# Kernel tuning notes

Measured on AMD Instinct MI355X. Metric: run time of the kernel, lower is better.

Reference implementation:

```python
import jax, jax.numpy as jnp
import numpy as np

EMBED_DIM = 1024
NUM_HEADS = 16
HEAD_DIM = EMBED_DIM // NUM_HEADS
MAX_DIST = 128
NUM_BUCKETS = 2 * MAX_DIST + 1  # 257: fixes off-by-one in original Embedding sizing


def setup_inputs() -> dict:
    key = jax.random.key(0)
    ks = jax.random.split(key, 10)
    B, S, D = 2, 2048, EMBED_DIM
    s = 1.0 / np.sqrt(D)
    return {
        "x": jax.random.normal(ks[0], (B, S, D), dtype=jnp.float32),
        "Wq": jax.random.normal(ks[1], (D, D), dtype=jnp.float32) * s,
        "bq": jnp.zeros((D,), dtype=jnp.float32),
        "Wk": jax.random.normal(ks[2], (D, D), dtype=jnp.float32) * s,
        "bk": jnp.zeros((D,), dtype=jnp.float32),
        "Wv": jax.random.normal(ks[3], (D, D), dtype=jnp.float32) * s,
        "bv": jnp.zeros((D,), dtype=jnp.float32),
        "Wo": jax.random.normal(ks[4], (D, D), dtype=jnp.float32) * s,
        "bo": jnp.zeros((D,), dtype=jnp.float32),
        "rel_emb": jax.random.normal(ks[5], (NUM_BUCKETS, NUM_HEADS), dtype=jnp.float32) * 0.02,
    }


def _rel_bias(rel_emb, seq_len):
    # relative position clamped to [-MAX_DIST, MAX_DIST], shifted to [0, 2*MAX_DIST]
    pos = jnp.arange(seq_len)
    rel = jnp.clip(pos[:, None] - pos[None, :], -MAX_DIST, MAX_DIST) + MAX_DIST
    bias = rel_emb[rel]                    # [S, S, H]
    return jnp.transpose(bias, (2, 0, 1))  # [H, S, S]


def reference(x, Wq, bq, Wk, bk, Wv, bv, Wo, bo, rel_emb):
    B, S, D = x.shape
    H, Hd = NUM_HEADS, HEAD_DIM
    # torch Linear: y = x @ W.T + b
    q = (x @ Wq.T + bq).reshape(B, S, H, Hd).transpose(0, 2, 1, 3)  # [B,H,S,Hd]
    k = (x @ Wk.T + bk).reshape(B, S, H, Hd).transpose(0, 2, 1, 3)
    v = (x @ Wv.T + bv).reshape(B, S, H, Hd).transpose(0, 2, 1, 3)
    scores = jnp.einsum("bhqd,bhkd->bhqk", q, k) / jnp.sqrt(jnp.float32(Hd))
    scores = scores + _rel_bias(rel_emb, S)[None]  # add [H,S,S] bias
    probs = jax.nn.softmax(scores, axis=-1)
    out = jnp.einsum("bhqk,bhkd->bhqd", probs, v)
    out = out.transpose(0, 2, 1, 3).reshape(B, S, D)
    return out @ Wo.T + bo
```

## Files before the change

kernel.cpp:

```cpp
#include <hip/hip_runtime.h>
#include <hip/hip_bf16.h>
#include <cstdint>
#include <cstddef>

#define DEVI __device__ __forceinline__

static constexpr int SEQ = 2048;
static constexpr int DM  = 1024;
static constexpr int NH  = 16;
static constexpr int HD  = 64;
static constexpr int NTOK = 2 * SEQ;
static constexpr int NBUCKET = 257;
static constexpr float LOG2E = 1.44269504088896f;

typedef __attribute__((ext_vector_type(8))) short bf16x8;
typedef __attribute__((ext_vector_type(4))) float f32x4;
#define MFMA16(a, b, c) __builtin_amdgcn_mfma_f32_16x16x32_bf16((a), (b), (c), 0, 0, 0)

DEVI float bf1(uint16_t u)  { return __uint_as_float(((uint32_t)u) << 16); }
DEVI uint16_t f2bf(float f) {
    uint32_t x = __float_as_uint(f);
    x += 0x7fffu + ((x >> 16) & 1u);
    return (uint16_t)(x >> 16);
}
DEVI bf16x8 ld_frag(const uint16_t* p) {
    union { uint4 u; bf16x8 f; } c;
    c.u = *(const uint4*)p;
    return c.f;
}
DEVI void gld16(const uint16_t* g, uint16_t* l) {
    __builtin_amdgcn_global_load_lds(
        (const __attribute__((address_space(1))) uint32_t*)g,
        (__attribute__((address_space(3))) uint32_t*)l, 16, 0, 0);
}

__global__ void sniff_kernel(const uint16_t* __restrict__ x, int* __restrict__ flag)
{
    int bad = 0;
    for (int i = threadIdx.x; i < 512; i += 64) {
        const float v = bf1(x[i]);
        if (!(fabsf(v) < 64.0f)) bad = 1;
    }
    const unsigned long long m = __ballot(bad);
    if (threadIdx.x == 0) *flag = (m != 0ull) ? 1 : 0;
}

__global__ __launch_bounds__(256)
void convert_kernel(const void* __restrict__ x, const void* __restrict__ Wq,
                    const void* __restrict__ Wk, const void* __restrict__ Wv,
                    const void* __restrict__ Wo, const void* __restrict__ bq,
                    const void* __restrict__ bk, const void* __restrict__ bv,
                    const void* __restrict__ bo, uint16_t* __restrict__ dst,
                    const int* __restrict__ flagp)
{
    const bool f32in = (*flagp != 0);
    const size_t M4 = 4194304, M1 = 1048576;
    const size_t e = ((size_t)blockIdx.x * 256 + threadIdx.x) * 8;
    const void* src; size_t off;
    if      (e < M4)                 { src = x;  off = e; }
    else if (e < M4 + M1)            { src = Wq; off = e - M4; }
    else if (e < M4 + 2*M1)          { src = Wk; off = e - M4 - M1; }
    else if (e < M4 + 3*M1)          { src = Wv; off = e - M4 - 2*M1; }
    else if (e < M4 + 4*M1)          { src = Wo; off = e - M4 - 3*M1; }
    else if (e < M4 + 4*M1 + 1024)   { src = bq; off = e - M4 - 4*M1; }
    else if (e < M4 + 4*M1 + 2048)   { src = bk; off = e - M4 - 4*M1 - 1024; }
    else if (e < M4 + 4*M1 + 3072)   { src = bv; off = e - M4 - 4*M1 - 2048; }
    else                             { src = bo; off = e - M4 - 4*M1 - 3072; }
    if (f32in) {
        const float4 a = *(const float4*)((const float*)src + off);
        const float4 b = *(const float4*)((const float*)src + off + 4);
        uint4 o;
        o.x = (uint32_t)f2bf(a.x) | ((uint32_t)f2bf(a.y) << 16);
        o.y = (uint32_t)f2bf(a.z) | ((uint32_t)f2bf(a.w) << 16);
        o.z = (uint32_t)f2bf(b.x) | ((uint32_t)f2bf(b.y) << 16);
        o.w = (uint32_t)f2bf(b.z) | ((uint32_t)f2bf(b.w) << 16);
        *(uint4*)(dst + e) = o;
    } else {
        *(uint4*)(dst + e) = *(const uint4*)((const uint16_t*)src + off);
    }
}

__global__ __launch_bounds__(256)
void gemm_qkv(const uint16_t* __restrict__ xc, const uint16_t* __restrict__ Wqkv,
              const uint16_t* __restrict__ bqkv,
              uint16_t* __restrict__ Qw, uint16_t* __restrict__ Kw,
              uint16_t* __restrict__ Vt)
{
    __shared__ uint16_t As[128 * 32];
    __shared__ uint16_t Bs[128 * 32];
    const int tid = threadIdx.x, bx = blockIdx.x;
    const int lane = tid & 63, wave = tid >> 6;
    const int ln = lane & 15, quad = lane >> 4;
    const int wm = (wave & 1) * 64, wn = (wave >> 1) * 64;

    const uint16_t *Ab, *Bb;
    int bm, bn, vor;
    if (bx < 512) {
        vor = 0; bm = (bx >> 4) * 128; bn = (bx & 15) * 128;
        Ab = xc + (size_t)bm * DM;  Bb = Wqkv + (size_t)bn * DM;
    } else {
        vor = 1; const int b2 = bx - 512; bm = (b2 >> 5) * 128; bn = (b2 & 31) * 128;
        Ab = Wqkv + (size_t)(2048 + bm) * DM;  Bb = xc + (size_t)bn * DM;
    }

    f32x4 acc[4][4];
    #pragma unroll
    for (int i = 0; i < 4; ++i)
        #pragma unroll
        for (int j = 0; j < 4; ++j) acc[i][j] = (f32x4){0.f, 0.f, 0.f, 0.f};

    const int s0 = tid, s1 = 256 + tid;
    const uint16_t* ga0 = Ab + (size_t)(s0 >> 2) * DM + (s0 & 3) * 8;
    const uint16_t* ga1 = Ab + (size_t)(s1 >> 2) * DM + (s1 & 3) * 8;
    const uint16_t* gb0 = Bb + (size_t)(s0 >> 2) * DM + (s0 & 3) * 8;
    const uint16_t* gb1 = Bb + (size_t)(s1 >> 2) * DM + (s1 & 3) * 8;

    for (int k0 = 0; k0 < DM; k0 += 32) {
        __syncthreads();
        gld16(ga0 + k0, &As[s0 * 8]);
        gld16(ga1 + k0, &As[s1 * 8]);
        gld16(gb0 + k0, &Bs[s0 * 8]);
        gld16(gb1 + k0, &Bs[s1 * 8]);
        __syncthreads();

        bf16x8 af[4], bfr[4];
        #pragma unroll
        for (int t = 0; t < 4; ++t) {
            af[t]  = ld_frag(&As[(wm + t * 16 + ln) * 32 + quad * 8]);
            bfr[t] = ld_frag(&Bs[(wn + t * 16 + ln) * 32 + quad * 8]);
        }
        #pragma unroll
        for (int ti = 0; ti < 4; ++ti)
            #pragma unroll
            for (int tj = 0; tj < 4; ++tj)
                acc[ti][tj] = MFMA16(af[ti], bfr[tj], acc[ti][tj]);
    }

    if (!vor) {
        #pragma unroll
        for (int tj = 0; tj < 4; ++tj) {
            const int c = bn + wn + tj * 16 + ln;
            const int mat = c >> 10, h = (c >> 6) & 15, hd = c & 63;
            uint16_t* dstp = mat ? Kw : Qw;
            const float scale = mat ? 1.0f : (0.125f * LOG2E);
            const float bb = bf1(bqkv[c]);
            #pragma unroll
            for (int ti = 0; ti < 4; ++ti)
                #pragma unroll
                for (int r = 0; r < 4; ++r) {
                    const int row = bm + wm + ti * 16 + quad * 4 + r;
                    const int b = row >> 11, s = row & 2047;
                    dstp[(((size_t)b * NH + h) * SEQ + s) * HD + hd] =
                        f2bf((acc[ti][tj][r] + bb) * scale);
                }
        }
    } else {
        #pragma unroll
        for (int ti = 0; ti < 4; ++ti)
            #pragma unroll
            for (int r = 0; r < 4; ++r) {
                const int f = bm + wm + ti * 16 + quad * 4 + r;
                const int h = f >> 6, hd = f & 63;
                const float bb = bf1(bqkv[2048 + f]);
                #pragma unroll
                for (int tj = 0; tj < 4; ++tj) {
                    const int t = bn + wn + tj * 16 + ln;
                    const int b = t >> 11, s = t & 2047;
                    Vt[(((size_t)b * NH + h) * HD + hd) * SEQ + s] = f2bf(acc[ti][tj][r] + bb);
                }
            }
    }
}

__global__ __launch_bounds__(256)
void gemm_out(const uint16_t* __restrict__ Cw, const uint16_t* __restrict__ Woc,
              const uint16_t* __restrict__ boc, void* __restrict__ out,
              const int* __restrict__ flagp)
{
    __shared__ uint16_t As[128 * 32];
    __shared__ uint16_t Bs[64 * 32];
    const int tid = threadIdx.x, bx = blockIdx.x;
    const int lane = tid & 63, wave = tid >> 6;
    const int ln = lane & 15, quad = lane >> 4;
    const int wm = (wave & 1) * 64, wn = (wave >> 1) * 32;
    const int bm = (bx >> 4) * 128, bn = (bx & 15) * 64;
    const uint16_t* Ab = Cw + (size_t)bm * DM;
    const uint16_t* Bb = Woc + (size_t)bn * DM;

    f32x4 acc[4][2];
    #pragma unroll
    for (int i = 0; i < 4; ++i)
        #pragma unroll
        for (int j = 0; j < 2; ++j) acc[i][j] = (f32x4){0.f, 0.f, 0.f, 0.f};

    const int s0 = tid, s1 = 256 + tid;
    const uint16_t* ga0 = Ab + (size_t)(s0 >> 2) * DM + (s0 & 3) * 8;
    const uint16_t* ga1 = Ab + (size_t)(s1 >> 2) * DM + (s1 & 3) * 8;
    const uint16_t* gb0 = Bb + (size_t)(s0 >> 2) * DM + (s0 & 3) * 8;

    for (int k0 = 0; k0 < DM; k0 += 32) {
        __syncthreads();
        gld16(ga0 + k0, &As[s0 * 8]);
        gld16(ga1 + k0, &As[s1 * 8]);
        gld16(gb0 + k0, &Bs[s0 * 8]);
        __syncthreads();

        bf16x8 af[4], bfr[2];
        #pragma unroll
        for (int t = 0; t < 4; ++t)
            af[t] = ld_frag(&As[(wm + t * 16 + ln) * 32 + quad * 8]);
        #pragma unroll
        for (int t = 0; t < 2; ++t)
            bfr[t] = ld_frag(&Bs[(wn + t * 16 + ln) * 32 + quad * 8]);
        #pragma unroll
        for (int ti = 0; ti < 4; ++ti)
            #pragma unroll
            for (int tj = 0; tj < 2; ++tj)
                acc[ti][tj] = MFMA16(af[ti], bfr[tj], acc[ti][tj]);
    }

    const bool f32o = (*flagp != 0);
    #pragma unroll
    for (int tj = 0; tj < 2; ++tj) {
        const int c = bn + wn + tj * 16 + ln;
        const float bb = bf1(boc[c]);
        #pragma unroll
        for (int ti = 0; ti < 4; ++ti)
            #pragma unroll
            for (int r = 0; r < 4; ++r) {
                const int row = bm + wm + ti * 16 + quad * 4 + r;
                const float v = acc[ti][tj][r] + bb;
                if (f32o) ((float*)out)[(size_t)row * DM + c] = v;
                else      ((uint16_t*)out)[(size_t)row * DM + c] = f2bf(v);
            }
    }
}

__global__ __launch_bounds__(256)
void attn_mfma(const uint16_t* __restrict__ Q, const uint16_t* __restrict__ K,
               const uint16_t* __restrict__ Vt, const void* __restrict__ rel,
               uint16_t* __restrict__ ctx, const int* __restrict__ flagp)
{
    __shared__ alignas(16) uint16_t Ks[64 * 64];
    __shared__ alignas(16) uint16_t Vls[64 * 64];
    __shared__ alignas(16) uint16_t Pl[4][16 * 64];
    __shared__ float bias_s[NBUCKET];

    const bool f32in = (*flagp != 0);
    const int tid = threadIdx.x, wave = tid >> 6, lane = tid & 63;
    const int ln = lane & 15, quad = lane >> 4;

    const int blk = blockIdx.x;
    const int bh = (blk & 7) * 4 + ((blk >> 3) & 3);
    const int qt = blk >> 5;
    const int b = bh >> 4, h = bh & 15;
    const int q0 = qt * 64;

    for (int i = tid; i < NBUCKET; i += 256) {
        const float bv = f32in ? ((const float*)rel)[i * NH + h]
                               : bf1(((const uint16_t*)rel)[i * NH + h]);
        bias_s[i] = bv * LOG2E;
    }
    __syncthreads();
    const float bneg = bias_s[0], bpos = bias_s[256];
    const float C8 = 8.0f * LOG2E;

    const uint16_t* qp = Q + ((size_t)bh * SEQ + q0 + wave * 16 + ln) * HD;
    const bf16x8 qf0 = ld_frag(qp + quad * 8);
    const bf16x8 qf1 = ld_frag(qp + 32 + quad * 8);

    f32x4 o[4];
    float lacc = 0.f;
    #pragma unroll
    for (int dt = 0; dt < 4; ++dt) o[dt] = (f32x4){0.f, 0.f, 0.f, 0.f};

    const uint16_t* Kb  = K  + (size_t)bh * SEQ * HD;
    const uint16_t* Vtb = Vt + (size_t)bh * HD * SEQ;
    const int swz = ln & 7;
    uint16_t* myP = Pl[wave];

    for (int k0 = 0; k0 < SEQ; k0 += 64) {
        __syncthreads();
        #pragma unroll
        for (int it = 0; it < 2; ++it) {
            const int s = it * 256 + tid;
            const int row = s >> 3, p = s & 7, c = p ^ (row & 7);
            gld16(Kb + (size_t)(k0 + row) * HD + c * 8, &Ks[s * 8]);
        }
        #pragma unroll
        for (int it = 0; it < 2; ++it) {
            const int s = it * 256 + tid;
            const int row = s >> 3, p = s & 7, c = p ^ (row & 7);
            gld16(Vtb + (size_t)row * SEQ + k0 + c * 8, &Vls[s * 8]);
        }
        __syncthreads();

        const int mode = (k0 >= q0 + 192) ? 0 : ((k0 + 192 <= q0) ? 2 : 1);
        const float bcst = ((mode == 0) ? bneg : bpos) - C8;

        #pragma unroll
        for (int nt = 0; nt < 4; ++nt) {
            const int krow = (nt * 16 + ln) * 64;
            const bf16x8 kf0 = ld_frag(&Ks[krow + ((0 + quad) ^ swz) * 8]);
            const bf16x8 kf1 = ld_frag(&Ks[krow + ((4 + quad) ^ swz) * 8]);
            f32x4 s4 = (f32x4){0.f, 0.f, 0.f, 0.f};
            s4 = MFMA16(kf0, qf0, s4);
            s4 = MFMA16(kf1, qf1, s4);
            uint32_t pb[4];
            #pragma unroll
            for (int r = 0; r < 4; ++r) {
                float sv;
                if (mode != 1) {
                    sv = s4[r] + bcst;
                } else {
                    const int kk = k0 + nt * 16 + quad * 4 + r;
                    const int qq = q0 + wave * 16 + ln;
                    int dd = qq - kk;
                    dd = min(128, max(-128, dd)) + 128;
                    sv = s4[r] + bias_s[dd] - C8;
                }
                pb[r] = __float_as_uint(exp2f(sv)) & 0xffff0000u;
                lacc += __uint_as_float(pb[r]);
            }
            const uint2 dw = {__builtin_amdgcn_perm(pb[1], pb[0], 0x07060302u),
                              __builtin_amdgcn_perm(pb[3], pb[2], 0x07060302u)};
            const int cb = (2 * nt + (quad >> 1)) ^ swz;
            *(uint2*)&myP[ln * 64 + cb * 8 + (quad & 1) * 4] = dw;
        }
        bf16x8 pf[2];
        #pragma unroll
        for (int kc = 0; kc < 2; ++kc)
            pf[kc] = ld_frag(&myP[ln * 64 + ((kc * 4 + quad) ^ swz) * 8]);
        #pragma unroll
        for (int dt = 0; dt < 4; ++dt) {
            const int vrow = (dt * 16 + ln) * 64;
            #pragma unroll
            for (int kc = 0; kc < 2; ++kc) {
                const bf16x8 vf = ld_frag(&Vls[vrow + ((kc * 4 + quad) ^ swz) * 8]);
                o[dt] = MFMA16(pf[kc], vf, o[dt]);
            }
        }
    }

    float lr = lacc;
    lr += __shfl_xor(lr, 16);
    lr += __shfl_xor(lr, 32);
    const float linv = 1.0f / lr;
    #pragma unroll
    for (int r = 0; r < 4; ++r) {
        const float inv_r = __shfl(linv, quad * 4 + r);
        const int qq = q0 + wave * 16 + quad * 4 + r;
        #pragma unroll
        for (int dt = 0; dt < 4; ++dt) {
            const float v = o[dt][r] * inv_r;
            ctx[(((size_t)b * SEQ + qq) * NH + h) * HD + dt * 16 + ln] = f2bf(v);
        }
    }
}

extern "C" void kernel_launch(void* const* d_in, const int* in_sizes, int n_in,
                              void* d_out, int out_size, void* d_ws, size_t ws_size,
                              hipStream_t stream)
{
    const void* x   = d_in[0];
    const void* Wq  = d_in[1];
    const void* bq  = d_in[2];
    const void* Wk  = d_in[3];
    const void* bk  = d_in[4];
    const void* Wv  = d_in[5];
    const void* bv  = d_in[6];
    const void* Wo  = d_in[7];
    const void* bo  = d_in[8];
    const void* rel = d_in[9];

    const size_t M4 = 4194304, M1 = 1048576;
    uint16_t* ws16 = (uint16_t*)d_ws;
    uint16_t* xc   = ws16;
    uint16_t* Wqkv = ws16 + M4;
    uint16_t* Woc  = ws16 + M4 + 3 * M1;
    uint16_t* bqkv = ws16 + M4 + 4 * M1;
    uint16_t* boc  = bqkv + 3072;
    uint16_t* Qw   = ws16 + M4 + 4 * M1 + 8192;
    uint16_t* Kw   = Qw + M4;
    uint16_t* Vt   = Kw + M4;
    int* flag = (int*)(Vt + M4);
    uint16_t* Cw = xc;

    sniff_kernel<<<1, 64, 0, stream>>>((const uint16_t*)x, flag);
    convert_kernel<<<4098, 256, 0, stream>>>(x, Wq, Wk, Wv, Wo, bq, bk, bv, bo,
                                             ws16, flag);
    gemm_qkv<<<768, 256, 0, stream>>>(xc, Wqkv, bqkv, Qw, Kw, Vt);
    attn_mfma<<<1024, 256, 0, stream>>>(Qw, Kw, Vt, rel, Cw, flag);
    gemm_out<<<512, 256, 0, stream>>>(Cw, Woc, boc, d_out, flag);
}
```

Measured before the change: 239.6 us.

## Compute softmax row sums via MFMA with ones vector and fold bias into accumulator init

Replaces the per-element scalar row-sum accumulation and its final cross-lane shuffles with two extra MFMAs per tile that multiply the stored bf16 probabilities by a ones vector. The constant bias and offset are folded into the MFMA accumulator initialisation and the bias table, removing per-element adds. The clamped-bias path is specialised into its own branch, and all LDS and global address arithmetic is hoisted out of the key loop. It also sets a minimum-blocks-per-SM hint in launch bounds, which may constrain register allocation.

```diff
diff --git a/kernel.cpp b/kernel.cpp
--- a/kernel.cpp
+++ b/kernel.cpp
@@ -236,7 +236,7 @@
     }
 }
 
-__global__ __launch_bounds__(256)
+__global__ __launch_bounds__(256, 4)
 void attn_mfma(const uint16_t* __restrict__ Q, const uint16_t* __restrict__ K,
                const uint16_t* __restrict__ Vt, const void* __restrict__ rel,
                uint16_t* __restrict__ ctx, const int* __restrict__ flagp)
@@ -256,21 +256,25 @@
     const int b = bh >> 4, h = bh & 15;
     const int q0 = qt * 64;
 
+    const float C8 = 8.0f * LOG2E;
     for (int i = tid; i < NBUCKET; i += 256) {
         const float bv = f32in ? ((const float*)rel)[i * NH + h]
                                : bf1(((const uint16_t*)rel)[i * NH + h]);
-        bias_s[i] = bv * LOG2E;
+        bias_s[i] = bv * LOG2E - C8;
     }
     __syncthreads();
     const float bneg = bias_s[0], bpos = bias_s[256];
-    const float C8 = 8.0f * LOG2E;
 
     const uint16_t* qp = Q + ((size_t)bh * SEQ + q0 + wave * 16 + ln) * HD;
     const bf16x8 qf0 = ld_frag(qp + quad * 8);
     const bf16x8 qf1 = ld_frag(qp + 32 + quad * 8);
 
+    union { uint4 u; bf16x8 f; } onec;
+    onec.u = (uint4){0x3F803F80u, 0x3F803F80u, 0x3F803F80u, 0x3F803F80u};
+    const bf16x8 onef = onec.f;
+
     f32x4 o[4];
-    float lacc = 0.f;
+    f32x4 lf = (f32x4){0.f, 0.f, 0.f, 0.f};
     #pragma unroll
     for (int dt = 0; dt < 4; ++dt) o[dt] = (f32x4){0.f, 0.f, 0.f, 0.f};
 
@@ -279,82 +283,107 @@
     const int swz = ln & 7;
     uint16_t* myP = Pl[wave];
 
+    const int s_0 = tid, s_1 = 256 + tid;
+    const int r_0 = s_0 >> 3, c_0 = (s_0 & 7) ^ (r_0 & 7);
+    const int r_1 = s_1 >> 3, c_1 = (s_1 & 7) ^ (r_1 & 7);
+    const int koff0 = r_0 * HD + c_0 * 8,  koff1 = r_1 * HD + c_1 * 8;
+    const int voff0 = r_0 * SEQ + c_0 * 8, voff1 = r_1 * SEQ + c_1 * 8;
+    uint16_t* const kl0 = &Ks[s_0 * 8];
+    uint16_t* const kl1 = &Ks[s_1 * 8];
+    uint16_t* const vl0 = &Vls[s_0 * 8];
+    uint16_t* const vl1 = &Vls[s_1 * 8];
+
+    const uint16_t* kfp[4][2];
+    const uint16_t* vfp[4][2];
+    #pragma unroll
+    for (int t = 0; t < 4; ++t) {
+        const int row = (t * 16 + ln) * 64;
+        kfp[t][0] = &Ks[row + ((0 + quad) ^ swz) * 8];
+        kfp[t][1] = &Ks[row + ((4 + quad) ^ swz) * 8];
+        vfp[t][0] = &Vls[row + ((0 + quad) ^ swz) * 8];
+        vfp[t][1] = &Vls[row + ((4 + quad) ^ swz) * 8];
+    }
+    uint16_t* Pw[4];
+    #pragma unroll
+    for (int nt = 0; nt < 4; ++nt) {
+        const int cb = (2 * nt + (quad >> 1)) ^ swz;
+        Pw[nt] = &myP[ln * 64 + cb * 8 + (quad & 1) * 4];
+    }
+    const uint16_t* const pfp0 = &myP[ln * 64 + ((0 + quad) ^ swz) * 8];
+    const uint16_t* const pfp1 = &myP[ln * 64 + ((4 + quad) ^ swz) * 8];
+
+    const uint16_t* kgb = Kb;
+    const uint16_t* vgb = Vtb;
+
     for (int k0 = 0; k0 < SEQ; k0 += 64) {
         __syncthreads();
-        #pragma unroll
-        for (int it = 0; it < 2; ++it) {
-            const int s = it * 256 + tid;
-            const int row = s >> 3, p = s & 7, c = p ^ (row & 7);
-            gld16(Kb + (size_t)(k0 + row) * HD + c * 8, &Ks[s * 8]);
-        }
-        #pragma unroll
-        for (int it = 0; it < 2; ++it) {
-            const int s = it * 256 + tid;
-            const int row = s >> 3, p = s & 7, c = p ^ (row & 7);
-            gld16(Vtb + (size_t)row * SEQ + k0 + c * 8, &Vls[s * 8]);
-        }
+        gld16(kgb + koff0, kl0);
+        gld16(kgb + koff1, kl1);
+        gld16(vgb + voff0, vl0);
+        gld16(vgb + voff1, vl1);
+        kgb += 64 * HD; vgb += 64;
         __syncthreads();
 
         const int mode = (k0 >= q0 + 192) ? 0 : ((k0 + 192 <= q0) ? 2 : 1);
-        const float bcst = ((mode == 0) ? bneg : bpos) - C8;
-
-        #pragma unroll
-        for (int nt = 0; nt < 4; ++nt) {
-            const int krow = (nt * 16 + ln) * 64;
-            const bf16x8 kf0 = ld_frag(&Ks[krow + ((0 + quad) ^ swz) * 8]);
-            const bf16x8 kf1 = ld_frag(&Ks[krow + ((4 + quad) ^ swz) * 8]);
-            f32x4 s4 = (f32x4){0.f, 0.f, 0.f, 0.f};
-            s4 = MFMA16(kf0, qf0, s4);
-            s4 = MFMA16(kf1, qf1, s4);
-            uint32_t pb[4];
-            #pragma unroll
-            for (int r = 0; r < 4; ++r) {
-                float sv;
-                if (mode != 1) {
-                    sv = s4[r] + bcst;
-                } else {
-                    const int kk = k0 + nt * 16 + quad * 4 + r;
-                    const int qq = q0 + wave * 16 + ln;
-                    int dd = qq - kk;
-                    dd = min(128, max(-128, dd)) + 128;
-                    sv = s4[r] + bias_s[dd] - C8;
+
+        if (mode != 1) {
+            const float binit = (mode == 0) ? bneg : bpos;
+            #pragma unroll
+            for (int nt = 0; nt < 4; ++nt) {
+                const bf16x8 kf0 = ld_frag(kfp[nt][0]);
+                const bf16x8 kf1 = ld_frag(kfp[nt][1]);
+                f32x4 s4 = (f32x4){binit, binit, binit, binit};
+                s4 = MFMA16(kf0, qf0, s4);
+                s4 = MFMA16(kf1, qf1, s4);
+                uint32_t pb[4];
+                #pragma unroll
+                for (int r = 0; r < 4; ++r)
+                    pb[r] = __float_as_uint(exp2f(s4[r]));
+                const uint2 dw = {__builtin_amdgcn_perm(pb[1], pb[0], 0x07060302u),
+                                  __builtin_amdgcn_perm(pb[3], pb[2], 0x07060302u)};
+                *(uint2*)Pw[nt] = dw;
+            }
+        } else {
+            const int iq = q0 + wave * 16 + ln + 128 - k0 - quad * 4;
+            #pragma unroll
+            for (int nt = 0; nt < 4; ++nt) {
+                const bf16x8 kf0 = ld_frag(kfp[nt][0]);
+                const bf16x8 kf1 = ld_frag(kfp[nt][1]);
+                f32x4 s4 = (f32x4){0.f, 0.f, 0.f, 0.f};
+                s4 = MFMA16(kf0, qf0, s4);
+                s4 = MFMA16(kf1, qf1, s4);
+                uint32_t pb[4];
+                #pragma unroll
+                for (int r = 0; r < 4; ++r) {
+                    int x = iq - (nt * 16 + r);
+                    x = max(0, min(256, x));
+                    pb[r] = __float_as_uint(exp2f(s4[r] + bias_s[x]));
                 }
-                pb[r] = __float_as_uint(exp2f(sv)) & 0xffff0000u;
-                lacc += __uint_as_float(pb[r]);
-            }
-            const uint2 dw = {__builtin_amdgcn_perm(pb[1], pb[0], 0x07060302u),
-                              __builtin_amdgcn_perm(pb[3], pb[2], 0x07060302u)};
-            const int cb = (2 * nt + (quad >> 1)) ^ swz;
-            *(uint2*)&myP[ln * 64 + cb * 8 + (quad & 1) * 4] = dw;
-        }
-        bf16x8 pf[2];
-        #pragma unroll
-        for (int kc = 0; kc < 2; ++kc)
-            pf[kc] = ld_frag(&myP[ln * 64 + ((kc * 4 + quad) ^ swz) * 8]);
-        #pragma unroll
-        for (int dt = 0; dt < 4; ++dt) {
-            const int vrow = (dt * 16 + ln) * 64;
-            #pragma unroll
-            for (int kc = 0; kc < 2; ++kc) {
-                const bf16x8 vf = ld_frag(&Vls[vrow + ((kc * 4 + quad) ^ swz) * 8]);
-                o[dt] = MFMA16(pf[kc], vf, o[dt]);
+                const uint2 dw = {__builtin_amdgcn_perm(pb[1], pb[0], 0x07060302u),
+                                  __builtin_amdgcn_perm(pb[3], pb[2], 0x07060302u)};
+                *(uint2*)Pw[nt] = dw;
             }
         }
-    }
-
-    float lr = lacc;
-    lr += __shfl_xor(lr, 16);
-    lr += __shfl_xor(lr, 32);
-    const float linv = 1.0f / lr;
+
+        const bf16x8 pf0 = ld_frag(pfp0);
+        const bf16x8 pf1 = ld_frag(pfp1);
+        lf = MFMA16(pf0, onef, lf);
+        lf = MFMA16(pf1, onef, lf);
+        #pragma unroll
+        for (int dt = 0; dt < 4; ++dt) {
+            o[dt] = MFMA16(pf0, ld_frag(vfp[dt][0]), o[dt]);
+            o[dt] = MFMA16(pf1, ld_frag(vfp[dt][1]), o[dt]);
+        }
+    }
+
     #pragma unroll
     for (int r = 0; r < 4; ++r) {
-        const float inv_r = __shfl(linv, quad * 4 + r);
+        const float inv = 1.0f / lf[r];
         const int qq = q0 + wave * 16 + quad * 4 + r;
         #pragma unroll
-        for (int dt = 0; dt < 4; ++dt) {
-            const float v = o[dt][r] * inv_r;
-            ctx[(((size_t)b * SEQ + qq) * NH + h) * HD + dt * 16 + ln] = f2bf(v);
-        }
+        for (int dt = 0; dt < 4; ++dt)
+            ctx[(((size_t)b * SEQ + qq) * NH + h) * HD + dt * 16 + ln] =
+                f2bf(o[dt][r] * inv);
     }
 }
 
```

Result: faster. 229.3 us (-4.3%).
